# Kernel optimization log

Measured on AMD Instinct MI355X. Metric: run time of the kernel, lower is better.

## Reference

```python
import jax, jax.numpy as jnp
import numpy as np

N_NODES = 100000
N_EDGES = 1600000
IN_CH = 512
HID_CH = 256
OUT_CH = 32
K = 10


def setup_inputs() -> dict:
    key = jax.random.key(0)
    k_x, k_e, k_w1, k_b1, k_w2, k_b2 = jax.random.split(key, 6)
    x = jax.random.normal(k_x, (N_NODES, IN_CH), dtype=jnp.float32)
    edge_index = jax.random.randint(k_e, (2, N_EDGES), 0, N_NODES, dtype=jnp.int64)
    s1 = 1.0 / np.sqrt(IN_CH)
    s2 = 1.0 / np.sqrt(HID_CH)
    W1 = jax.random.uniform(k_w1, (IN_CH, HID_CH), jnp.float32, -s1, s1)
    b1 = jax.random.uniform(k_b1, (HID_CH,), jnp.float32, -s1, s1)
    W2 = jax.random.uniform(k_w2, (HID_CH, OUT_CH), jnp.float32, -s2, s2)
    b2 = jax.random.uniform(k_b2, (OUT_CH,), jnp.float32, -s2, s2)
    gamma = jnp.ones((K + 1,), jnp.float32) / (K + 1)
    return {"x": x, "edge_index": edge_index, "W1": W1, "b1": b1,
            "W2": W2, "b2": b2, "gamma": gamma}


def reference(x, edge_index, W1, b1, W2, b2, gamma):
    # MLP (dropout is identity in eval mode)
    h = jax.nn.relu(x @ W1 + b1) @ W2 + b2  # [N, out]
    row, col = edge_index[0], edge_index[1]
    # symmetric normalization: deg over destination nodes (col)
    deg = jax.ops.segment_sum(jnp.ones((N_EDGES,), h.dtype), col,
                              num_segments=N_NODES)
    deg_inv_sqrt = jnp.where(deg > 0, jax.lax.rsqrt(jnp.maximum(deg, 1.0)), 0.0)
    norm = (deg_inv_sqrt[row] * deg_inv_sqrt[col])[:, None]  # [E, 1]
    out = gamma[0] * h
    h_k = h
    for k in range(1, K + 1):
        # one hop: gather source feats, scale, scatter-add to destinations
        h_k = jax.ops.segment_sum(norm * h_k[row], col, num_segments=N_NODES)
        out = out + gamma[k] * h_k
    return out
```

## Files before the change

### kernel.cpp

```cpp
#include <hip/hip_runtime.h>
#include <hip/hip_bf16.h>

#define NN    100000
#define NE    1600000
#define INCH  512
#define HIDCH 256
#define OUTCH 32
#define KHOPS 10

typedef __attribute__((ext_vector_type(8))) short short8;
typedef __attribute__((ext_vector_type(4))) float f32x4;

#define GLOAD_LDS16(gsrc, ldst) \
  __builtin_amdgcn_global_load_lds((const __attribute__((address_space(1))) void*)(gsrc), \
                                   (__attribute__((address_space(3))) void*)(ldst), 16, 0, 0)

constexpr size_t ws_align(size_t x) { return (x + 255) & ~(size_t)255; }
constexpr size_t OFF_H1   = 0;
constexpr size_t OFF_HA   = OFF_H1   + ws_align((size_t)NN*HIDCH*2);
constexpr size_t OFF_HB   = OFF_HA   + ws_align((size_t)NN*OUTCH*2);
constexpr size_t OFF_W1TH = OFF_HB   + ws_align((size_t)NN*OUTCH*2);
constexpr size_t OFF_W1TL = OFF_W1TH + ws_align((size_t)HIDCH*INCH*2);
constexpr size_t OFF_W2TH = OFF_W1TL + ws_align((size_t)HIDCH*INCH*2);
constexpr size_t OFF_W2TL = OFF_W2TH + ws_align((size_t)OUTCH*HIDCH*2);
constexpr size_t OFF_DEG  = OFF_W2TL + ws_align((size_t)OUTCH*HIDCH*2);
constexpr size_t OFF_DIS  = OFF_DEG  + ws_align((size_t)NN*4);
constexpr size_t OFF_RP   = OFF_DIS  + ws_align((size_t)NN*4);
constexpr size_t OFF_CUR  = OFF_RP   + ws_align((size_t)(NN+1)*4);
constexpr size_t OFF_EPK  = OFF_CUR  + ws_align((size_t)NN*4);
constexpr size_t OFF_PART = OFF_EPK  + ws_align((size_t)NE*8);
constexpr size_t OFF_OFFS = OFF_PART + ws_align(512);

__device__ __forceinline__ unsigned short bf16_rne(float f) {
  unsigned int u = __float_as_uint(f);
  u += 0x7fffu + ((u >> 16) & 1u);
  return (unsigned short)(u >> 16);
}
__device__ __forceinline__ float bf16_to_f32(unsigned short h) {
  return __uint_as_float(((unsigned int)h) << 16);
}

__global__ __launch_bounds__(256) void k_count_deg(const int* __restrict__ col,
                                                   int* __restrict__ deg) {
  int e = blockIdx.x * 256 + threadIdx.x;
  if (e < NE) atomicAdd(&deg[col[e]], 1);
}

__global__ __launch_bounds__(256) void k_dis(const int* __restrict__ deg,
                                             float* __restrict__ dis) {
  int v = blockIdx.x * 256 + threadIdx.x;
  if (v < NN) {
    int d = deg[v];
    dis[v] = d > 0 ? rsqrtf((float)d) : 0.0f;
  }
}

__global__ __launch_bounds__(256) void k_scan1(const int* __restrict__ deg,
                                               int* __restrict__ rp,
                                               int* __restrict__ part) {
  __shared__ int s[256];
  int b = blockIdx.x, t = threadIdx.x;
  int base = b * 1024 + t * 4;
  int v0 = (base + 0 < NN) ? deg[base + 0] : 0;
  int v1 = (base + 1 < NN) ? deg[base + 1] : 0;
  int v2 = (base + 2 < NN) ? deg[base + 2] : 0;
  int v3 = (base + 3 < NN) ? deg[base + 3] : 0;
  int tot = v0 + v1 + v2 + v3;
  s[t] = tot;
  __syncthreads();
  for (int d = 1; d < 256; d <<= 1) {
    int x = (t >= d) ? s[t - d] : 0;
    __syncthreads();
    s[t] += x;
    __syncthreads();
  }
  int excl = s[t] - tot;
  if (t == 255) part[b] = s[255];
  if (base + 0 < NN) rp[base + 0] = excl;
  if (base + 1 < NN) rp[base + 1] = excl + v0;
  if (base + 2 < NN) rp[base + 2] = excl + v0 + v1;
  if (base + 3 < NN) rp[base + 3] = excl + v0 + v1 + v2;
}

__global__ __launch_bounds__(128) void k_scan2(const int* __restrict__ part,
                                               int* __restrict__ offs) {
  __shared__ int s[128];
  int t = threadIdx.x;
  int v = (t < 98) ? part[t] : 0;
  s[t] = v;
  __syncthreads();
  for (int d = 1; d < 128; d <<= 1) {
    int x = (t >= d) ? s[t - d] : 0;
    __syncthreads();
    s[t] += x;
    __syncthreads();
  }
  if (t < 98) offs[t] = s[t] - v;
}

__global__ __launch_bounds__(256) void k_scan3(int* __restrict__ rp,
                                               const int* __restrict__ offs,
                                               int* __restrict__ cur) {
  int b = blockIdx.x, t = threadIdx.x;
  int o = offs[b];
  int base = b * 1024 + t * 4;
#pragma unroll
  for (int j = 0; j < 4; ++j) {
    int i = base + j;
    if (i < NN) {
      int r = rp[i] + o;
      rp[i] = r;
      cur[i] = r;
    }
  }
  if (b == 0 && t == 0) rp[NN] = NE;
}

__global__ __launch_bounds__(256) void k_fill(const int* __restrict__ ei,
                                              const float* __restrict__ dis,
                                              int* __restrict__ cur,
                                              int2* __restrict__ epk) {
  int e = blockIdx.x * 256 + threadIdx.x;
  if (e < NE) {
    int r = ei[e], c = ei[NE + e];
    int p = atomicAdd(&cur[c], 1);
    epk[p] = make_int2(r, __float_as_int(dis[r] * dis[c]));
  }
}

__global__ __launch_bounds__(256) void k_splitT(const float* __restrict__ src,
                                                unsigned short* __restrict__ dh,
                                                unsigned short* __restrict__ dl,
                                                int K, int N) {
  int idx = blockIdx.x * 256 + threadIdx.x;
  if (idx >= K * N) return;
  int n = idx / K, k = idx - n * K;
  float v = src[(size_t)k * N + n];
  unsigned short h = bf16_rne(v);
  dh[idx] = h;
  dl[idx] = bf16_rne(v - bf16_to_f32(h));
}

__global__ __launch_bounds__(512, 2) void k_gemm1(const float* __restrict__ X,
                                                  const unsigned short* __restrict__ W1Th,
                                                  const unsigned short* __restrict__ W1Tl,
                                                  const float* __restrict__ bias1,
                                                  unsigned short* __restrict__ H1bf) {
  __shared__ __align__(16) unsigned short Ah[2][4096];
  __shared__ __align__(16) unsigned short Bh[2][8192], Bl[2][8192];
  const int t = threadIdx.x;
  const int m0 = blockIdx.x * 128;
  const int w = t >> 6, lane = t & 63;
  const int wm = w >> 2, wn = w & 3;

  const int arow = t >> 2;
  const int achk = t & 3;
  int axrow = m0 + arow; if (axrow >= NN) axrow = NN - 1;
  const float* aptr = X + (size_t)axrow * INCH + achk * 8;
  int aidx = (arow >> 4) * 512 + ((arow & 15) + achk * 16) * 8;
  aidx ^= ((aidx >> 7) & 3) << 4;
  const int aroff = (lane * 8) ^ (((lane >> 4) & 3) << 4);

  const int bn0 = (w * 16) + (lane & 15);
  const int bko = (lane >> 4) * 8;
  const unsigned short* bs0 = W1Th + (size_t)bn0 * INCH + bko;
  const unsigned short* bs1 = W1Th + (size_t)(bn0 + 128) * INCH + bko;
  const unsigned short* bs2 = W1Tl + (size_t)bn0 * INCH + bko;
  const unsigned short* bs3 = W1Tl + (size_t)(bn0 + 128) * INCH + bko;

  f32x4 acc[4][4] = {};
  float4 av0, av1;

  av0 = *(const float4*)(aptr);
  av1 = *(const float4*)(aptr + 4);
  GLOAD_LDS16(bs0, &Bh[0][w * 512]);
  GLOAD_LDS16(bs1, &Bh[0][(w + 8) * 512]);
  GLOAD_LDS16(bs2, &Bl[0][w * 512]);
  GLOAD_LDS16(bs3, &Bl[0][(w + 8) * 512]);
  {
    float af[8] = {av0.x, av0.y, av0.z, av0.w, av1.x, av1.y, av1.z, av1.w};
    short8 ah;
#pragma unroll
    for (int i = 0; i < 8; ++i) {
      unsigned int u = __float_as_uint(af[i]);
      ah[i] = (short)((u + 0x7fffu + ((u >> 16) & 1u)) >> 16);
    }
    *(short8*)&Ah[0][aidx] = ah;
  }
  __syncthreads();

#pragma unroll
  for (int it = 0; it < 16; ++it) {
    const int cur = it & 1, nxt = cur ^ 1;
    const int k0 = it * 32;
    if (it < 15) {
      av0 = *(const float4*)(aptr + k0 + 32);
      av1 = *(const float4*)(aptr + k0 + 36);
      GLOAD_LDS16(bs0 + k0 + 32, &Bh[nxt][w * 512]);
      GLOAD_LDS16(bs1 + k0 + 32, &Bh[nxt][(w + 8) * 512]);
      GLOAD_LDS16(bs2 + k0 + 32, &Bl[nxt][w * 512]);
      GLOAD_LDS16(bs3 + k0 + 32, &Bl[nxt][(w + 8) * 512]);
    }
    short8 afrag[4];
#pragma unroll
    for (int mf = 0; mf < 4; ++mf)
      afrag[mf] = *(const short8*)&Ah[cur][(wm * 4 + mf) * 512 + aroff];
#pragma unroll
    for (int nf = 0; nf < 4; ++nf) {
      short8 bfh = *(const short8*)&Bh[cur][(wn * 4 + nf) * 512 + lane * 8];
      short8 bfl = *(const short8*)&Bl[cur][(wn * 4 + nf) * 512 + lane * 8];
#pragma unroll
      for (int mf = 0; mf < 4; ++mf) {
        acc[mf][nf] = __builtin_amdgcn_mfma_f32_16x16x32_bf16(afrag[mf], bfh, acc[mf][nf], 0, 0, 0);
        acc[mf][nf] = __builtin_amdgcn_mfma_f32_16x16x32_bf16(afrag[mf], bfl, acc[mf][nf], 0, 0, 0);
      }
    }
    if (it < 15) {
      float af[8] = {av0.x, av0.y, av0.z, av0.w, av1.x, av1.y, av1.z, av1.w};
      short8 ah;
#pragma unroll
      for (int i = 0; i < 8; ++i) {
        unsigned int u = __float_as_uint(af[i]);
        ah[i] = (short)((u + 0x7fffu + ((u >> 16) & 1u)) >> 16);
      }
      *(short8*)&Ah[nxt][aidx] = ah;
    }
    __syncthreads();
  }

  const int colbase = wn * 64 + (lane & 15);
  const int rowbase = m0 + wm * 64 + ((lane >> 4) << 2);
#pragma unroll
  for (int nf = 0; nf < 4; ++nf) {
    int col = colbase + nf * 16;
    float b = bias1[col];
#pragma unroll
    for (int mf = 0; mf < 4; ++mf) {
#pragma unroll
      for (int r = 0; r < 4; ++r) {
        int row = rowbase + mf * 16 + r;
        if (row < NN) {
          float h = fmaxf(acc[mf][nf][r] + b, 0.f);
          H1bf[(size_t)row * HIDCH + col] = bf16_rne(h);
        }
      }
    }
  }
}

__global__ __launch_bounds__(256) void k_gemm2(const unsigned short* __restrict__ H1bf,
                                               const unsigned short* __restrict__ W2Th,
                                               const unsigned short* __restrict__ W2Tl,
                                               const float* __restrict__ bias2,
                                               const float* __restrict__ gamma,
                                               unsigned short* __restrict__ hA,
                                               float* __restrict__ out) {
  __shared__ __align__(16) unsigned short A2[8192];
  __shared__ __align__(16) unsigned short B2h[2048], B2l[2048];
  const int t = threadIdx.x;
  const int m0 = blockIdx.x * 128;

  const int arow = t >> 1;
  int axrow = m0 + arow; if (axrow >= NN) axrow = NN - 1;
  const int akb = (t & 1) * 32;
  const unsigned short* ap = H1bf + (size_t)axrow * HIDCH + akb;
  const int abase = ((arow >> 4) * 2 + (akb >> 5)) * 512 + (arow & 15) * 8;

  const int bnr = t >> 3, bkq = (t & 7) * 8;
  const int bslot = ((bnr >> 4) * 2 + (bkq >> 5)) * 512 +
                    ((bnr & 15) + (((bkq & 31) >> 3) << 4)) * 8;
  const unsigned short* bhp = W2Th + (size_t)bnr * HIDCH + bkq;
  const unsigned short* blp = W2Tl + (size_t)bnr * HIDCH + bkq;

  const int w = t >> 6, lane = t & 63;

  f32x4 acc[2][2] = {};

  for (int k0 = 0; k0 < HIDCH; k0 += 64) {
    uint4 a0 = *(const uint4*)(ap + k0);
    uint4 a1 = *(const uint4*)(ap + k0 + 8);
    uint4 a2 = *(const uint4*)(ap + k0 + 16);
    uint4 a3 = *(const uint4*)(ap + k0 + 24);
    uint4 bh = *(const uint4*)(bhp + k0);
    uint4 bl = *(const uint4*)(blp + k0);

    __syncthreads();

    *(uint4*)&A2[abase + 0 * 128] = a0;
    *(uint4*)&A2[abase + 1 * 128] = a1;
    *(uint4*)&A2[abase + 2 * 128] = a2;
    *(uint4*)&A2[abase + 3 * 128] = a3;
    *(uint4*)&B2h[bslot] = bh;
    *(uint4*)&B2l[bslot] = bl;

    __syncthreads();

    const short8* AV  = (const short8*)A2;
    const short8* BHV = (const short8*)B2h;
    const short8* BLV = (const short8*)B2l;
#pragma unroll
    for (int k32 = 0; k32 < 2; ++k32) {
      short8 bfh[2], bfl[2];
#pragma unroll
      for (int nf = 0; nf < 2; ++nf) {
        bfh[nf] = BHV[(nf * 2 + k32) * 64 + lane];
        bfl[nf] = BLV[(nf * 2 + k32) * 64 + lane];
      }
#pragma unroll
      for (int mf = 0; mf < 2; ++mf) {
        short8 a = AV[((w * 2 + mf) * 2 + k32) * 64 + lane];
#pragma unroll
        for (int nf = 0; nf < 2; ++nf) {
          acc[mf][nf] = __builtin_amdgcn_mfma_f32_16x16x32_bf16(a, bfh[nf], acc[mf][nf], 0, 0, 0);
          acc[mf][nf] = __builtin_amdgcn_mfma_f32_16x16x32_bf16(a, bfl[nf], acc[mf][nf], 0, 0, 0);
        }
      }
    }
  }

  const float g0 = gamma[0];
  const int colb = lane & 15;
  const int rowb = m0 + w * 32 + ((lane >> 4) << 2);
#pragma unroll
  for (int nf = 0; nf < 2; ++nf) {
    int col = nf * 16 + colb;
    float b = bias2[col];
#pragma unroll
    for (int mf = 0; mf < 2; ++mf) {
#pragma unroll
      for (int r = 0; r < 4; ++r) {
        int row = rowb + mf * 16 + r;
        if (row < NN) {
          float h = acc[mf][nf][r] + b;
          hA[(size_t)row * OUTCH + col] = bf16_rne(h);
          out[(size_t)row * OUTCH + col] = g0 * h;
        }
      }
    }
  }
}

__global__ __launch_bounds__(256) void k_hop(const unsigned short* __restrict__ hin,
                                             unsigned short* __restrict__ hout,
                                             float* __restrict__ out,
                                             const int* __restrict__ rp,
                                             const int2* __restrict__ epk,
                                             const float* __restrict__ gamma,
                                             int k) {
  __shared__ int2 meta[8][32];
  const int hw = threadIdx.x >> 5;
  const int c  = threadIdx.x & 31;
  const int v  = blockIdx.x * 8 + hw;
  const int s = rp[v], e = rp[v + 1];
  float acc0 = 0.f, acc1 = 0.f, acc2 = 0.f, acc3 = 0.f;
  for (int base = s; base < e; base += 32) {
    const int cnt = min(32, e - base);
    if (c < cnt) meta[hw][c] = epk[base + c];
    int j = 0;
    for (; j + 4 <= cnt; j += 4) {
      int4 q0 = *(const int4*)&meta[hw][j];
      int4 q1 = *(const int4*)&meta[hw][j + 2];
      float v0 = bf16_to_f32(hin[(size_t)q0.x * OUTCH + c]);
      float v1 = bf16_to_f32(hin[(size_t)q0.z * OUTCH + c]);
      float v2 = bf16_to_f32(hin[(size_t)q1.x * OUTCH + c]);
      float v3 = bf16_to_f32(hin[(size_t)q1.z * OUTCH + c]);
      acc0 = fmaf(__int_as_float(q0.y), v0, acc0);
      acc1 = fmaf(__int_as_float(q0.w), v1, acc1);
      acc2 = fmaf(__int_as_float(q1.y), v2, acc2);
      acc3 = fmaf(__int_as_float(q1.w), v3, acc3);
    }
    for (; j < cnt; ++j) {
      int2 m = meta[hw][j];
      acc0 = fmaf(__int_as_float(m.y), bf16_to_f32(hin[(size_t)m.x * OUTCH + c]), acc0);
    }
  }
  float tot = (acc0 + acc1) + (acc2 + acc3);
  hout[(size_t)v * OUTCH + c] = bf16_rne(tot);
  out[(size_t)v * OUTCH + c] += gamma[k] * tot;
}

extern "C" void kernel_launch(void* const* d_in, const int* in_sizes, int n_in,
                              void* d_out, int out_size, void* d_ws, size_t ws_size,
                              hipStream_t stream) {
  const float* x     = (const float*)d_in[0];
  const int*   ei    = (const int*)d_in[1];
  const float* W1    = (const float*)d_in[2];
  const float* b1    = (const float*)d_in[3];
  const float* W2    = (const float*)d_in[4];
  const float* b2    = (const float*)d_in[5];
  const float* gamma = (const float*)d_in[6];
  float* out = (float*)d_out;

  char* ws = (char*)d_ws;
  unsigned short* h1bf = (unsigned short*)(ws + OFF_H1);
  unsigned short* hA   = (unsigned short*)(ws + OFF_HA);
  unsigned short* hB   = (unsigned short*)(ws + OFF_HB);
  unsigned short* w1th = (unsigned short*)(ws + OFF_W1TH);
  unsigned short* w1tl = (unsigned short*)(ws + OFF_W1TL);
  unsigned short* w2th = (unsigned short*)(ws + OFF_W2TH);
  unsigned short* w2tl = (unsigned short*)(ws + OFF_W2TL);
  int*   deg  = (int*)(ws + OFF_DEG);
  float* dis  = (float*)(ws + OFF_DIS);
  int*   rp   = (int*)(ws + OFF_RP);
  int*   cur  = (int*)(ws + OFF_CUR);
  int2*  epk  = (int2*)(ws + OFF_EPK);
  int*   part = (int*)(ws + OFF_PART);
  int*   offs = (int*)(ws + OFF_OFFS);

  hipMemsetAsync(deg, 0, NN * sizeof(int), stream);

  k_splitT<<<(INCH * HIDCH + 255) / 256, 256, 0, stream>>>(W1, w1th, w1tl, INCH, HIDCH);
  k_splitT<<<(HIDCH * OUTCH + 255) / 256, 256, 0, stream>>>(W2, w2th, w2tl, HIDCH, OUTCH);

  k_count_deg<<<(NE + 255) / 256, 256, 0, stream>>>(ei + NE, deg);
  k_dis<<<(NN + 255) / 256, 256, 0, stream>>>(deg, dis);
  k_scan1<<<98, 256, 0, stream>>>(deg, rp, part);
  k_scan2<<<1, 128, 0, stream>>>(part, offs);
  k_scan3<<<98, 256, 0, stream>>>(rp, offs, cur);
  k_fill<<<(NE + 255) / 256, 256, 0, stream>>>(ei, dis, cur, epk);

  k_gemm1<<<(NN + 127) / 128, 512, 0, stream>>>(x, w1th, w1tl, b1, h1bf);
  k_gemm2<<<(NN + 127) / 128, 256, 0, stream>>>(h1bf, w2th, w2tl, b2, gamma, hA, out);

  unsigned short* hin = hA;
  unsigned short* hout = hB;
  for (int k = 1; k <= KHOPS; ++k) {
    k_hop<<<NN / 8, 256, 0, stream>>>(hin, hout, out, rp, epk, gamma, k);
    unsigned short* tmp = hin; hin = hout; hout = tmp;
  }
}
```

Measured before the change: 625.0 us.

## Deepen gemm1 X prefetch pipeline and switch hop features to fp32 with float2 gathers

The first GEMM now prefetches X two K-steps ahead into register double buffers. It uses explicit vmcnt waits, scheduling barriers and split barriers so global loads overlap the MFMA work. The propagation hops store intermediate features in fp32 instead of bf16. Each node is handled by 16 lanes doing float2 gathers, with 16 nodes per block. This halves lane work per edge and removes bf16 rounding error, but doubles the bytes gathered per hop.

```diff
diff --git a/kernel.cpp b/kernel.cpp
--- a/kernel.cpp
+++ b/kernel.cpp
@@ -15,11 +15,15 @@
   __builtin_amdgcn_global_load_lds((const __attribute__((address_space(1))) void*)(gsrc), \
                                    (__attribute__((address_space(3))) void*)(ldst), 16, 0, 0)
 
+#define WAIT_VM(N) asm volatile("s_waitcnt vmcnt(" #N ")" ::: "memory")
+#define WAIT_LGKM0() asm volatile("s_waitcnt lgkmcnt(0)" ::: "memory")
+#define PIN() __builtin_amdgcn_sched_barrier(0)
+
 constexpr size_t ws_align(size_t x) { return (x + 255) & ~(size_t)255; }
 constexpr size_t OFF_H1   = 0;
 constexpr size_t OFF_HA   = OFF_H1   + ws_align((size_t)NN*HIDCH*2);
-constexpr size_t OFF_HB   = OFF_HA   + ws_align((size_t)NN*OUTCH*2);
-constexpr size_t OFF_W1TH = OFF_HB   + ws_align((size_t)NN*OUTCH*2);
+constexpr size_t OFF_HB   = OFF_HA   + ws_align((size_t)NN*OUTCH*4);
+constexpr size_t OFF_W1TH = OFF_HB   + ws_align((size_t)NN*OUTCH*4);
 constexpr size_t OFF_W1TL = OFF_W1TH + ws_align((size_t)HIDCH*INCH*2);
 constexpr size_t OFF_W2TH = OFF_W1TL + ws_align((size_t)HIDCH*INCH*2);
 constexpr size_t OFF_W2TL = OFF_W2TH + ws_align((size_t)OUTCH*HIDCH*2);
@@ -169,16 +173,20 @@
   const unsigned short* bs3 = W1Tl + (size_t)(bn0 + 128) * INCH + bko;
 
   f32x4 acc[4][4] = {};
-  float4 av0, av1;
-
-  av0 = *(const float4*)(aptr);
-  av1 = *(const float4*)(aptr + 4);
+  float4 rA0[2], rA1[2];
+
+  float4 p0 = *(const float4*)(aptr);
+  float4 p1 = *(const float4*)(aptr + 4);
+  rA0[1] = *(const float4*)(aptr + 32);
+  rA1[1] = *(const float4*)(aptr + 36);
   GLOAD_LDS16(bs0, &Bh[0][w * 512]);
   GLOAD_LDS16(bs1, &Bh[0][(w + 8) * 512]);
   GLOAD_LDS16(bs2, &Bl[0][w * 512]);
   GLOAD_LDS16(bs3, &Bl[0][(w + 8) * 512]);
+  PIN();
+  WAIT_VM(6);
   {
-    float af[8] = {av0.x, av0.y, av0.z, av0.w, av1.x, av1.y, av1.z, av1.w};
+    float af[8] = {p0.x, p0.y, p0.z, p0.w, p1.x, p1.y, p1.z, p1.w};
     short8 ah;
 #pragma unroll
     for (int i = 0; i < 8; ++i) {
@@ -187,20 +195,42 @@
     }
     *(short8*)&Ah[0][aidx] = ah;
   }
-  __syncthreads();
 
 #pragma unroll
   for (int it = 0; it < 16; ++it) {
     const int cur = it & 1, nxt = cur ^ 1;
-    const int k0 = it * 32;
+    if (it < 14) {
+      const int ka = (it + 2) * 32;
+      if (cur == 0) { rA0[0] = *(const float4*)(aptr + ka); rA1[0] = *(const float4*)(aptr + ka + 4); }
+      else          { rA0[1] = *(const float4*)(aptr + ka); rA1[1] = *(const float4*)(aptr + ka + 4); }
+    }
     if (it < 15) {
-      av0 = *(const float4*)(aptr + k0 + 32);
-      av1 = *(const float4*)(aptr + k0 + 36);
-      GLOAD_LDS16(bs0 + k0 + 32, &Bh[nxt][w * 512]);
-      GLOAD_LDS16(bs1 + k0 + 32, &Bh[nxt][(w + 8) * 512]);
-      GLOAD_LDS16(bs2 + k0 + 32, &Bl[nxt][w * 512]);
-      GLOAD_LDS16(bs3 + k0 + 32, &Bl[nxt][(w + 8) * 512]);
-    }
+      const int kb = (it + 1) * 32;
+      GLOAD_LDS16(bs0 + kb, &Bh[nxt][w * 512]);
+      GLOAD_LDS16(bs1 + kb, &Bh[nxt][(w + 8) * 512]);
+      GLOAD_LDS16(bs2 + kb, &Bl[nxt][w * 512]);
+      GLOAD_LDS16(bs3 + kb, &Bl[nxt][(w + 8) * 512]);
+    }
+    PIN();
+    if (it < 14)      WAIT_VM(6);
+    else if (it == 14) WAIT_VM(4);
+    else               WAIT_VM(0);
+    PIN();
+    if (it < 15) {
+      float4 qa = (nxt == 0) ? rA0[0] : rA0[1];
+      float4 qb = (nxt == 0) ? rA1[0] : rA1[1];
+      float af[8] = {qa.x, qa.y, qa.z, qa.w, qb.x, qb.y, qb.z, qb.w};
+      short8 ah;
+#pragma unroll
+      for (int i = 0; i < 8; ++i) {
+        unsigned int u = __float_as_uint(af[i]);
+        ah[i] = (short)((u + 0x7fffu + ((u >> 16) & 1u)) >> 16);
+      }
+      *(short8*)&Ah[nxt][aidx] = ah;
+    }
+    WAIT_LGKM0();
+    __builtin_amdgcn_s_barrier();
+    PIN();
     short8 afrag[4];
 #pragma unroll
     for (int mf = 0; mf < 4; ++mf)
@@ -215,17 +245,11 @@
         acc[mf][nf] = __builtin_amdgcn_mfma_f32_16x16x32_bf16(afrag[mf], bfl, acc[mf][nf], 0, 0, 0);
       }
     }
+    PIN();
     if (it < 15) {
-      float af[8] = {av0.x, av0.y, av0.z, av0.w, av1.x, av1.y, av1.z, av1.w};
-      short8 ah;
-#pragma unroll
-      for (int i = 0; i < 8; ++i) {
-        unsigned int u = __float_as_uint(af[i]);
-        ah[i] = (short)((u + 0x7fffu + ((u >> 16) & 1u)) >> 16);
-      }
-      *(short8*)&Ah[nxt][aidx] = ah;
-    }
-    __syncthreads();
+      __builtin_amdgcn_s_barrier();
+      PIN();
+    }
   }
 
   const int colbase = wn * 64 + (lane & 15);
@@ -253,7 +277,7 @@
                                                const unsigned short* __restrict__ W2Tl,
                                                const float* __restrict__ bias2,
                                                const float* __restrict__ gamma,
-                                               unsigned short* __restrict__ hA,
+                                               float* __restrict__ hA,
                                                float* __restrict__ out) {
   __shared__ __align__(16) unsigned short A2[8192];
   __shared__ __align__(16) unsigned short B2h[2048], B2l[2048];
@@ -332,7 +356,7 @@
         int row = rowb + mf * 16 + r;
         if (row < NN) {
           float h = acc[mf][nf][r] + b;
-          hA[(size_t)row * OUTCH + col] = bf16_rne(h);
+          hA[(size_t)row * OUTCH + col] = h;
           out[(size_t)row * OUTCH + col] = g0 * h;
         }
       }
@@ -340,43 +364,48 @@
   }
 }
 
-__global__ __launch_bounds__(256) void k_hop(const unsigned short* __restrict__ hin,
-                                             unsigned short* __restrict__ hout,
+__global__ __launch_bounds__(256) void k_hop(const float* __restrict__ hin,
+                                             float* __restrict__ hout,
                                              float* __restrict__ out,
                                              const int* __restrict__ rp,
                                              const int2* __restrict__ epk,
                                              const float* __restrict__ gamma,
                                              int k) {
-  __shared__ int2 meta[8][32];
-  const int hw = threadIdx.x >> 5;
-  const int c  = threadIdx.x & 31;
-  const int v  = blockIdx.x * 8 + hw;
+  __shared__ int2 meta[16][20];
+  const int t = threadIdx.x;
+  const int q = t >> 4;
+  const int c2 = t & 15;
+  const int v = blockIdx.x * 16 + q;
   const int s = rp[v], e = rp[v + 1];
-  float acc0 = 0.f, acc1 = 0.f, acc2 = 0.f, acc3 = 0.f;
-  for (int base = s; base < e; base += 32) {
-    const int cnt = min(32, e - base);
-    if (c < cnt) meta[hw][c] = epk[base + c];
-    int j = 0;
-    for (; j + 4 <= cnt; j += 4) {
-      int4 q0 = *(const int4*)&meta[hw][j];
-      int4 q1 = *(const int4*)&meta[hw][j + 2];
-      float v0 = bf16_to_f32(hin[(size_t)q0.x * OUTCH + c]);
-      float v1 = bf16_to_f32(hin[(size_t)q0.z * OUTCH + c]);
-      float v2 = bf16_to_f32(hin[(size_t)q1.x * OUTCH + c]);
-      float v3 = bf16_to_f32(hin[(size_t)q1.z * OUTCH + c]);
-      acc0 = fmaf(__int_as_float(q0.y), v0, acc0);
-      acc1 = fmaf(__int_as_float(q0.w), v1, acc1);
-      acc2 = fmaf(__int_as_float(q1.y), v2, acc2);
-      acc3 = fmaf(__int_as_float(q1.w), v3, acc3);
-    }
-    for (; j < cnt; ++j) {
-      int2 m = meta[hw][j];
-      acc0 = fmaf(__int_as_float(m.y), bf16_to_f32(hin[(size_t)m.x * OUTCH + c]), acc0);
-    }
-  }
-  float tot = (acc0 + acc1) + (acc2 + acc3);
-  hout[(size_t)v * OUTCH + c] = bf16_rne(tot);
-  out[(size_t)v * OUTCH + c] += gamma[k] * tot;
+  float ax0 = 0.f, ay0 = 0.f, ax1 = 0.f, ay1 = 0.f;
+  float ax2 = 0.f, ay2 = 0.f, ax3 = 0.f, ay3 = 0.f;
+  for (int base = s; base < e; base += 16) {
+    const int cnt = min(16, e - base);
+    int2 m = (c2 < cnt) ? epk[base + c2] : make_int2(0, 0);
+    meta[q][c2] = m;
+    const int steps = (cnt + 3) >> 2;
+    for (int j = 0; j < steps; ++j) {
+      int4 e01 = *(const int4*)&meta[q][j * 4];
+      int4 e23 = *(const int4*)&meta[q][j * 4 + 2];
+      float2 g0 = *(const float2*)&hin[(size_t)e01.x * OUTCH + c2 * 2];
+      float2 g1 = *(const float2*)&hin[(size_t)e01.z * OUTCH + c2 * 2];
+      float2 g2 = *(const float2*)&hin[(size_t)e23.x * OUTCH + c2 * 2];
+      float2 g3 = *(const float2*)&hin[(size_t)e23.z * OUTCH + c2 * 2];
+      float n0 = __int_as_float(e01.y), n1 = __int_as_float(e01.w);
+      float n2 = __int_as_float(e23.y), n3 = __int_as_float(e23.w);
+      ax0 = fmaf(n0, g0.x, ax0); ay0 = fmaf(n0, g0.y, ay0);
+      ax1 = fmaf(n1, g1.x, ax1); ay1 = fmaf(n1, g1.y, ay1);
+      ax2 = fmaf(n2, g2.x, ax2); ay2 = fmaf(n2, g2.y, ay2);
+      ax3 = fmaf(n3, g3.x, ax3); ay3 = fmaf(n3, g3.y, ay3);
+    }
+  }
+  const float tx = (ax0 + ax1) + (ax2 + ax3);
+  const float ty = (ay0 + ay1) + (ay2 + ay3);
+  const size_t o = (size_t)v * OUTCH + c2 * 2;
+  *(float2*)&hout[o] = make_float2(tx, ty);
+  const float g = gamma[k];
+  float2 po = *(const float2*)&out[o];
+  *(float2*)&out[o] = make_float2(fmaf(g, tx, po.x), fmaf(g, ty, po.y));
 }
 
 extern "C" void kernel_launch(void* const* d_in, const int* in_sizes, int n_in,
@@ -393,8 +422,8 @@
 
   char* ws = (char*)d_ws;
   unsigned short* h1bf = (unsigned short*)(ws + OFF_H1);
-  unsigned short* hA   = (unsigned short*)(ws + OFF_HA);
-  unsigned short* hB   = (unsigned short*)(ws + OFF_HB);
+  float* hA   = (float*)(ws + OFF_HA);
+  float* hB   = (float*)(ws + OFF_HB);
   unsigned short* w1th = (unsigned short*)(ws + OFF_W1TH);
   unsigned short* w1tl = (unsigned short*)(ws + OFF_W1TL);
   unsigned short* w2th = (unsigned short*)(ws + OFF_W2TH);
@@ -422,10 +451,10 @@
   k_gemm1<<<(NN + 127) / 128, 512, 0, stream>>>(x, w1th, w1tl, b1, h1bf);
   k_gemm2<<<(NN + 127) / 128, 256, 0, stream>>>(h1bf, w2th, w2tl, b2, gamma, hA, out);
 
-  unsigned short* hin = hA;
-  unsigned short* hout = hB;
+  float* hin = hA;
+  float* hout = hB;
   for (int k = 1; k <= KHOPS; ++k) {
-    k_hop<<<NN / 8, 256, 0, stream>>>(hin, hout, out, rp, epk, gamma, k);
-    unsigned short* tmp = hin; hin = hout; hout = tmp;
-  }
-}
+    k_hop<<<NN / 16, 256, 0, stream>>>(hin, hout, out, rp, epk, gamma, k);
+    float* tmp = hin; hin = hout; hout = tmp;
+  }
+}
```

New measurement: 666.9 us. 6.7% more time.

## Prescale features by inverse degree, split channels into halves, pad CSR to 4

Applied to the files above, without the earlier changes.

The per-edge weight dis[r]*dis[c] is folded into node features: the stored features are pre-multiplied by dis, and each hop multiplies by dis squared. The edge list then holds only source indices, which halves edge metadata traffic. Channels are split into two 16-wide halves, each propagated by its own hop kernel, so every source row gather is a 32-byte segment that may stay cache-resident. CSR rows are padded to multiples of 4 with a zero sentinel node so the inner loop needs no tail handling. The costs are twice as many hop launches, an extra pad kernel, a final merge kernel, and slightly different bf16 rounding from the prescaling.

```diff
diff --git a/kernel.cpp b/kernel.cpp
--- a/kernel.cpp
+++ b/kernel.cpp
@@ -7,6 +7,7 @@
 #define HIDCH 256
 #define OUTCH 32
 #define KHOPS 10
+#define NEPAD (NE + 3 * NN)
 
 typedef __attribute__((ext_vector_type(8))) short short8;
 typedef __attribute__((ext_vector_type(4))) float f32x4;
@@ -16,10 +17,16 @@
                                    (__attribute__((address_space(3))) void*)(ldst), 16, 0, 0)
 
 constexpr size_t ws_align(size_t x) { return (x + 255) & ~(size_t)255; }
+constexpr size_t USZ = ws_align((size_t)(NN + 1) * 16 * 2);
+constexpr size_t OSZ = ws_align((size_t)NN * 16 * 4);
 constexpr size_t OFF_H1   = 0;
-constexpr size_t OFF_HA   = OFF_H1   + ws_align((size_t)NN*HIDCH*2);
-constexpr size_t OFF_HB   = OFF_HA   + ws_align((size_t)NN*OUTCH*2);
-constexpr size_t OFF_W1TH = OFF_HB   + ws_align((size_t)NN*OUTCH*2);
+constexpr size_t OFF_U00  = OFF_H1   + ws_align((size_t)NN*HIDCH*2);
+constexpr size_t OFF_U01  = OFF_U00  + USZ;
+constexpr size_t OFF_U10  = OFF_U01  + USZ;
+constexpr size_t OFF_U11  = OFF_U10  + USZ;
+constexpr size_t OFF_OA0  = OFF_U11  + USZ;
+constexpr size_t OFF_OA1  = OFF_OA0  + OSZ;
+constexpr size_t OFF_W1TH = OFF_OA1  + OSZ;
 constexpr size_t OFF_W1TL = OFF_W1TH + ws_align((size_t)HIDCH*INCH*2);
 constexpr size_t OFF_W2TH = OFF_W1TL + ws_align((size_t)HIDCH*INCH*2);
 constexpr size_t OFF_W2TL = OFF_W2TH + ws_align((size_t)OUTCH*HIDCH*2);
@@ -27,8 +34,8 @@
 constexpr size_t OFF_DIS  = OFF_DEG  + ws_align((size_t)NN*4);
 constexpr size_t OFF_RP   = OFF_DIS  + ws_align((size_t)NN*4);
 constexpr size_t OFF_CUR  = OFF_RP   + ws_align((size_t)(NN+1)*4);
-constexpr size_t OFF_EPK  = OFF_CUR  + ws_align((size_t)NN*4);
-constexpr size_t OFF_PART = OFF_EPK  + ws_align((size_t)NE*8);
+constexpr size_t OFF_CSR  = OFF_CUR  + ws_align((size_t)NN*4);
+constexpr size_t OFF_PART = OFF_CSR  + ws_align((size_t)NEPAD*4);
 constexpr size_t OFF_OFFS = OFF_PART + ws_align(512);
 
 __device__ __forceinline__ unsigned short bf16_rne(float f) {
@@ -47,11 +54,20 @@
 }
 
 __global__ __launch_bounds__(256) void k_dis(const int* __restrict__ deg,
-                                             float* __restrict__ dis) {
+                                             float* __restrict__ dis,
+                                             unsigned short* u00, unsigned short* u01,
+                                             unsigned short* u10, unsigned short* u11) {
   int v = blockIdx.x * 256 + threadIdx.x;
   if (v < NN) {
     int d = deg[v];
     dis[v] = d > 0 ? rsqrtf((float)d) : 0.0f;
+  }
+  if (blockIdx.x == 0) {
+    int t = threadIdx.x;
+    if (t < 8)       ((unsigned int*)u00)[(size_t)NN * 8 + t] = 0;
+    else if (t < 16) ((unsigned int*)u01)[(size_t)NN * 8 + (t - 8)] = 0;
+    else if (t < 24) ((unsigned int*)u10)[(size_t)NN * 8 + (t - 16)] = 0;
+    else if (t < 32) ((unsigned int*)u11)[(size_t)NN * 8 + (t - 24)] = 0;
   }
 }
 
@@ -61,10 +77,10 @@
   __shared__ int s[256];
   int b = blockIdx.x, t = threadIdx.x;
   int base = b * 1024 + t * 4;
-  int v0 = (base + 0 < NN) ? deg[base + 0] : 0;
-  int v1 = (base + 1 < NN) ? deg[base + 1] : 0;
-  int v2 = (base + 2 < NN) ? deg[base + 2] : 0;
-  int v3 = (base + 3 < NN) ? deg[base + 3] : 0;
+  int v0 = (base + 0 < NN) ? ((deg[base + 0] + 3) & ~3) : 0;
+  int v1 = (base + 1 < NN) ? ((deg[base + 1] + 3) & ~3) : 0;
+  int v2 = (base + 2 < NN) ? ((deg[base + 2] + 3) & ~3) : 0;
+  int v3 = (base + 3 < NN) ? ((deg[base + 3] + 3) & ~3) : 0;
   int tot = v0 + v1 + v2 + v3;
   s[t] = tot;
   __syncthreads();
@@ -100,6 +116,7 @@
 
 __global__ __launch_bounds__(256) void k_scan3(int* __restrict__ rp,
                                                const int* __restrict__ offs,
+                                               const int* __restrict__ part,
                                                int* __restrict__ cur) {
   int b = blockIdx.x, t = threadIdx.x;
   int o = offs[b];
@@ -113,18 +130,27 @@
       cur[i] = r;
     }
   }
-  if (b == 0 && t == 0) rp[NN] = NE;
+  if (b == 0 && t == 0) rp[NN] = offs[97] + part[97];
 }
 
 __global__ __launch_bounds__(256) void k_fill(const int* __restrict__ ei,
-                                              const float* __restrict__ dis,
                                               int* __restrict__ cur,
-                                              int2* __restrict__ epk) {
+                                              int* __restrict__ csrc) {
   int e = blockIdx.x * 256 + threadIdx.x;
   if (e < NE) {
-    int r = ei[e], c = ei[NE + e];
+    int c = ei[NE + e];
     int p = atomicAdd(&cur[c], 1);
-    epk[p] = make_int2(r, __float_as_int(dis[r] * dis[c]));
+    csrc[p] = ei[e];
+  }
+}
+
+__global__ __launch_bounds__(256) void k_pad(const int* __restrict__ cur,
+                                             const int* __restrict__ rp,
+                                             int* __restrict__ csrc) {
+  int v = blockIdx.x * 256 + threadIdx.x;
+  if (v < NN) {
+    int p = cur[v], e = rp[v + 1];
+    for (; p < e; ++p) csrc[p] = NN;
   }
 }
 
@@ -253,8 +279,11 @@
                                                const unsigned short* __restrict__ W2Tl,
                                                const float* __restrict__ bias2,
                                                const float* __restrict__ gamma,
-                                               unsigned short* __restrict__ hA,
-                                               float* __restrict__ out) {
+                                               const float* __restrict__ dis,
+                                               unsigned short* __restrict__ u00,
+                                               unsigned short* __restrict__ u01,
+                                               float* __restrict__ oa0,
+                                               float* __restrict__ oa1) {
   __shared__ __align__(16) unsigned short A2[8192];
   __shared__ __align__(16) unsigned short B2h[2048], B2l[2048];
   const int t = threadIdx.x;
@@ -321,62 +350,85 @@
   const float g0 = gamma[0];
   const int colb = lane & 15;
   const int rowb = m0 + w * 32 + ((lane >> 4) << 2);
-#pragma unroll
-  for (int nf = 0; nf < 2; ++nf) {
-    int col = nf * 16 + colb;
-    float b = bias2[col];
-#pragma unroll
-    for (int mf = 0; mf < 2; ++mf) {
-#pragma unroll
-      for (int r = 0; r < 4; ++r) {
-        int row = rowb + mf * 16 + r;
-        if (row < NN) {
-          float h = acc[mf][nf][r] + b;
-          hA[(size_t)row * OUTCH + col] = bf16_rne(h);
-          out[(size_t)row * OUTCH + col] = g0 * h;
-        }
-      }
-    }
-  }
-}
-
-__global__ __launch_bounds__(256) void k_hop(const unsigned short* __restrict__ hin,
-                                             unsigned short* __restrict__ hout,
-                                             float* __restrict__ out,
+  const float b2c0 = bias2[colb], b2c1 = bias2[16 + colb];
+#pragma unroll
+  for (int mf = 0; mf < 2; ++mf) {
+#pragma unroll
+    for (int r = 0; r < 4; ++r) {
+      int row = rowb + mf * 16 + r;
+      if (row < NN) {
+        float dv = dis[row];
+        float h0 = acc[mf][0][r] + b2c0;
+        float h1 = acc[mf][1][r] + b2c1;
+        size_t o = (size_t)row * 16 + colb;
+        u00[o] = bf16_rne(dv * h0);
+        u01[o] = bf16_rne(dv * h1);
+        oa0[o] = g0 * h0;
+        oa1[o] = g0 * h1;
+      }
+    }
+  }
+}
+
+__global__ __launch_bounds__(256) void k_hop(const unsigned short* __restrict__ Uin,
+                                             unsigned short* __restrict__ Uout,
+                                             float* __restrict__ oacc,
                                              const int* __restrict__ rp,
-                                             const int2* __restrict__ epk,
+                                             const int* __restrict__ csrc,
+                                             const float* __restrict__ dis,
                                              const float* __restrict__ gamma,
                                              int k) {
-  __shared__ int2 meta[8][32];
-  const int hw = threadIdx.x >> 5;
-  const int c  = threadIdx.x & 31;
-  const int v  = blockIdx.x * 8 + hw;
+  __shared__ int meta[32][36];
+  const int t = threadIdx.x;
+  const int g = t >> 3;
+  const int li = t & 7;
+  const int v = blockIdx.x * 32 + g;
   const int s = rp[v], e = rp[v + 1];
-  float acc0 = 0.f, acc1 = 0.f, acc2 = 0.f, acc3 = 0.f;
+  float ax0 = 0.f, ay0 = 0.f, ax1 = 0.f, ay1 = 0.f;
+  float ax2 = 0.f, ay2 = 0.f, ax3 = 0.f, ay3 = 0.f;
   for (int base = s; base < e; base += 32) {
+    const int idx0 = base + li * 4;
+    int4 mv = make_int4(NN, NN, NN, NN);
+    if (idx0 < e) mv = *(const int4*)&csrc[idx0];
+    *(int4*)&meta[g][li * 4] = mv;
     const int cnt = min(32, e - base);
-    if (c < cnt) meta[hw][c] = epk[base + c];
-    int j = 0;
-    for (; j + 4 <= cnt; j += 4) {
-      int4 q0 = *(const int4*)&meta[hw][j];
-      int4 q1 = *(const int4*)&meta[hw][j + 2];
-      float v0 = bf16_to_f32(hin[(size_t)q0.x * OUTCH + c]);
-      float v1 = bf16_to_f32(hin[(size_t)q0.z * OUTCH + c]);
-      float v2 = bf16_to_f32(hin[(size_t)q1.x * OUTCH + c]);
-      float v3 = bf16_to_f32(hin[(size_t)q1.z * OUTCH + c]);
-      acc0 = fmaf(__int_as_float(q0.y), v0, acc0);
-      acc1 = fmaf(__int_as_float(q0.w), v1, acc1);
-      acc2 = fmaf(__int_as_float(q1.y), v2, acc2);
-      acc3 = fmaf(__int_as_float(q1.w), v3, acc3);
-    }
-    for (; j < cnt; ++j) {
-      int2 m = meta[hw][j];
-      acc0 = fmaf(__int_as_float(m.y), bf16_to_f32(hin[(size_t)m.x * OUTCH + c]), acc0);
-    }
-  }
-  float tot = (acc0 + acc1) + (acc2 + acc3);
-  hout[(size_t)v * OUTCH + c] = bf16_rne(tot);
-  out[(size_t)v * OUTCH + c] += gamma[k] * tot;
+    const int nst = cnt >> 2;
+    for (int j = 0; j < nst; ++j) {
+      int4 sv = *(const int4*)&meta[g][j * 4];
+      unsigned int w0 = *(const unsigned int*)&Uin[(size_t)sv.x * 16 + li * 2];
+      unsigned int w1 = *(const unsigned int*)&Uin[(size_t)sv.y * 16 + li * 2];
+      unsigned int w2 = *(const unsigned int*)&Uin[(size_t)sv.z * 16 + li * 2];
+      unsigned int w3 = *(const unsigned int*)&Uin[(size_t)sv.w * 16 + li * 2];
+      ax0 += __uint_as_float(w0 << 16); ay0 += __uint_as_float(w0 & 0xffff0000u);
+      ax1 += __uint_as_float(w1 << 16); ay1 += __uint_as_float(w1 & 0xffff0000u);
+      ax2 += __uint_as_float(w2 << 16); ay2 += __uint_as_float(w2 & 0xffff0000u);
+      ax3 += __uint_as_float(w3 << 16); ay3 += __uint_as_float(w3 & 0xffff0000u);
+    }
+  }
+  const float Sx = (ax0 + ax1) + (ax2 + ax3);
+  const float Sy = (ay0 + ay1) + (ay2 + ay3);
+  const float dv = dis[v];
+  const float gd = gamma[k] * dv;
+  const float d2 = dv * dv;
+  unsigned int packed = (unsigned int)bf16_rne(d2 * Sx) |
+                        ((unsigned int)bf16_rne(d2 * Sy) << 16);
+  ((unsigned int*)Uout)[(size_t)v * 8 + li] = packed;
+  float2 po = *(const float2*)&oacc[(size_t)v * 16 + li * 2];
+  po.x = fmaf(gd, Sx, po.x);
+  po.y = fmaf(gd, Sy, po.y);
+  *(float2*)&oacc[(size_t)v * 16 + li * 2] = po;
+}
+
+__global__ __launch_bounds__(256) void k_merge(const float* __restrict__ oa0,
+                                               const float* __restrict__ oa1,
+                                               float* __restrict__ out) {
+  int i4 = blockIdx.x * 256 + threadIdx.x;
+  if (i4 >= NN * 8) return;
+  int v = i4 >> 3;
+  int j = (i4 & 7) * 4;
+  const float* src = (j < 16) ? oa0 : oa1;
+  float4 val = *(const float4*)&src[(size_t)v * 16 + (j & 15)];
+  *(float4*)&out[(size_t)v * 32 + j] = val;
 }
 
 extern "C" void kernel_launch(void* const* d_in, const int* in_sizes, int n_in,
@@ -393,8 +445,11 @@
 
   char* ws = (char*)d_ws;
   unsigned short* h1bf = (unsigned short*)(ws + OFF_H1);
-  unsigned short* hA   = (unsigned short*)(ws + OFF_HA);
-  unsigned short* hB   = (unsigned short*)(ws + OFF_HB);
+  unsigned short* U[2][2] = {
+    {(unsigned short*)(ws + OFF_U00), (unsigned short*)(ws + OFF_U01)},
+    {(unsigned short*)(ws + OFF_U10), (unsigned short*)(ws + OFF_U11)}};
+  float* oa0 = (float*)(ws + OFF_OA0);
+  float* oa1 = (float*)(ws + OFF_OA1);
   unsigned short* w1th = (unsigned short*)(ws + OFF_W1TH);
   unsigned short* w1tl = (unsigned short*)(ws + OFF_W1TL);
   unsigned short* w2th = (unsigned short*)(ws + OFF_W2TH);
@@ -403,7 +458,7 @@
   float* dis  = (float*)(ws + OFF_DIS);
   int*   rp   = (int*)(ws + OFF_RP);
   int*   cur  = (int*)(ws + OFF_CUR);
-  int2*  epk  = (int2*)(ws + OFF_EPK);
+  int*   csrc = (int*)(ws + OFF_CSR);
   int*   part = (int*)(ws + OFF_PART);
   int*   offs = (int*)(ws + OFF_OFFS);
 
@@ -413,19 +468,22 @@
   k_splitT<<<(HIDCH * OUTCH + 255) / 256, 256, 0, stream>>>(W2, w2th, w2tl, HIDCH, OUTCH);
 
   k_count_deg<<<(NE + 255) / 256, 256, 0, stream>>>(ei + NE, deg);
-  k_dis<<<(NN + 255) / 256, 256, 0, stream>>>(deg, dis);
+  k_dis<<<(NN + 255) / 256, 256, 0, stream>>>(deg, dis, U[0][0], U[0][1], U[1][0], U[1][1]);
   k_scan1<<<98, 256, 0, stream>>>(deg, rp, part);
   k_scan2<<<1, 128, 0, stream>>>(part, offs);
-  k_scan3<<<98, 256, 0, stream>>>(rp, offs, cur);
-  k_fill<<<(NE + 255) / 256, 256, 0, stream>>>(ei, dis, cur, epk);
+  k_scan3<<<98, 256, 0, stream>>>(rp, offs, part, cur);
+  k_fill<<<(NE + 255) / 256, 256, 0, stream>>>(ei, cur, csrc);
+  k_pad<<<(NN + 255) / 256, 256, 0, stream>>>(cur, rp, csrc);
 
   k_gemm1<<<(NN + 127) / 128, 512, 0, stream>>>(x, w1th, w1tl, b1, h1bf);
-  k_gemm2<<<(NN + 127) / 128, 256, 0, stream>>>(h1bf, w2th, w2tl, b2, gamma, hA, out);
-
-  unsigned short* hin = hA;
-  unsigned short* hout = hB;
+  k_gemm2<<<(NN + 127) / 128, 256, 0, stream>>>(h1bf, w2th, w2tl, b2, gamma, dis,
+                                                U[0][0], U[0][1], oa0, oa1);
+
   for (int k = 1; k <= KHOPS; ++k) {
-    k_hop<<<NN / 8, 256, 0, stream>>>(hin, hout, out, rp, epk, gamma, k);
-    unsigned short* tmp = hin; hin = hout; hout = tmp;
-  }
-}
+    const int pin = (k - 1) & 1, pout = k & 1;
+    k_hop<<<NN / 32, 256, 0, stream>>>(U[pin][0], U[pout][0], oa0, rp, csrc, dis, gamma, k);
+    k_hop<<<NN / 32, 256, 0, stream>>>(U[pin][1], U[pout][1], oa1, rp, csrc, dis, gamma, k);
+  }
+
+  k_merge<<<(NN * 8 + 255) / 256, 256, 0, stream>>>(oa0, oa1, out);
+}
```

New measurement: 645.2 us. +3.2%, slower.
